# Kernel optimization log

Hardware: AMD Instinct MI355X
Metric: run time of the kernel (lower is better)

Reference implementation:

```python
import jax, jax.numpy as jnp
import numpy as np

ALPHA = 0.2  # LeakyReLU negative slope
NEG_INF = -9e15


def make_quaternion_mul(kernel):
    # kernel: (in/4, out); returns hamilton: (in, out)
    r, i, j, k = jnp.split(kernel, 4, axis=1)
    r2 = jnp.concatenate([r, -i, -j, -k], axis=0)
    i2 = jnp.concatenate([i, r, -k, j], axis=0)
    j2 = jnp.concatenate([j, k, r, -i], axis=0)
    k2 = jnp.concatenate([k, -j, i, r], axis=0)
    return jnp.concatenate([r2, i2, j2, k2], axis=1)


def setup_inputs() -> dict:
    key = jax.random.key(0)
    k1, k2, k3, k4 = jax.random.split(key, 4)
    N, IN, OUT, H = 4096, 512, 128, 4
    x = jax.random.normal(k1, (N, IN), dtype=jnp.float32)
    adj = jax.random.randint(k2, (N, N), 0, 2, dtype=jnp.int32)
    stdv = float(np.sqrt(6.0 / (IN // 4 + OUT)))
    W = jax.random.uniform(k3, (H, IN // 4, OUT), dtype=jnp.float32,
                           minval=-stdv, maxval=stdv)
    a_std = float(np.sqrt(2.0 / (2 * OUT + 1))) * 1.414
    a = jax.random.normal(k4, (H, 2 * OUT), dtype=jnp.float32) * a_std
    return {"x": x, "adj": adj, "W": W, "a": a}


def reference(x, adj, W, a):
    N = x.shape[0]
    hamilton = jax.vmap(make_quaternion_mul)(W)          # (H, IN, OUT)
    h = jnp.einsum('nf,hfo->hno', x, hamilton)           # (H, N, OUT)
    OUT = h.shape[-1]
    a_src, a_dst = a[:, :OUT], a[:, OUT:]
    # e[h,i,j] = leakyrelu(h_i . a_src + h_j . a_dst), same math as repeat/cat
    f_src = jnp.einsum('hno,ho->hn', h, a_src)           # (H, N)
    f_dst = jnp.einsum('hno,ho->hn', h, a_dst)           # (H, N)
    e = jax.nn.leaky_relu(f_src[:, :, None] + f_dst[:, None, :], ALPHA)
    e = jnp.where((adj > 0)[None, :, :], e, NEG_INF)
    attn = jax.nn.softmax(e, axis=-1)                    # (H, N, N)
    # dropout p=0.0 / eval mode -> identity
    h_prime = jnp.einsum('hnm,hmo->hno', attn, h)        # (H, N, OUT)
    out = jnp.transpose(h_prime, (1, 0, 2)).reshape(N, -1)  # concat heads
    return jax.nn.elu(out)
```

## Files before the change

### kernel.cpp

```cpp
#include <hip/hip_runtime.h>
#include <math.h>

#define ALPHA 0.2f

#define XS   544
#define HS   4128
#define HCS  66048

typedef __attribute__((ext_vector_type(8))) short short8;
typedef __attribute__((ext_vector_type(4))) float f32x4;
typedef __attribute__((ext_vector_type(4))) int i32x4;

__device__ __forceinline__ unsigned short f2bf(float f) {
    unsigned int x = __float_as_uint(f);
    x += 0x7fffu + ((x >> 16) & 1u);
    return (unsigned short)(x >> 16);
}
__device__ __forceinline__ unsigned int pack_rne(float lo, float hi) {
    return (unsigned int)f2bf(lo) | ((unsigned int)f2bf(hi) << 16);
}
__device__ __forceinline__ unsigned int pack_trunc(float lo, float hi) {
    return __builtin_amdgcn_perm(__float_as_uint(hi), __float_as_uint(lo), 0x07060302u);
}
__device__ __forceinline__ unsigned int bitmask1(unsigned int x, int j) {
    return (unsigned int)(((int)(x << (31 - j))) >> 31);
}

__global__ __launch_bounds__(256) void k_prep(const float* __restrict__ x,
                                              const float* __restrict__ W,
                                              const int* __restrict__ adj,
                                              unsigned short* __restrict__ xbf,
                                              unsigned short* __restrict__ hamT,
                                              unsigned int* __restrict__ adjp32) {
    const int b = blockIdx.x;
    if (b < 1024) {
        const int gid = b * 256 + threadIdx.x;
        const int row = gid >> 6, c8 = (gid & 63) * 8;
        const float4* xp = (const float4*)x + (size_t)gid * 2;
        const float4 f0 = xp[0], f1 = xp[1];
        const uint4 o = {pack_rne(f0.x, f0.y), pack_rne(f0.z, f0.w),
                         pack_rne(f1.x, f1.y), pack_rne(f1.z, f1.w)};
        *(uint4*)(xbf + (size_t)row * XS + c8) = o;
    } else if (b < 1152) {
        const int gid = (b - 1024) * 256 + threadIdx.x;
        const int head = gid >> 13;
        const int rem  = gid & 8191;
        const int o = rem >> 6, f8 = rem & 63;
        const int ob = o >> 5, oc = o & 31;
        float v[8];
#pragma unroll
        for (int j = 0; j < 8; j++) {
            const int f = f8 * 8 + j;
            const int bq = f >> 7, f0 = f & 127;
            const float s = ((0x5390u >> ((bq << 2) | ob)) & 1u) ? -1.0f : 1.0f;
            v[j] = s * W[(head << 14) + (f0 << 7) + (((bq ^ ob) << 5) | oc)];
        }
        const uint4 pk = {pack_rne(v[0], v[1]), pack_rne(v[2], v[3]),
                          pack_rne(v[4], v[5]), pack_rne(v[6], v[7])};
        *(uint4*)(hamT + (size_t)(head * 128 + o) * XS + f8 * 8) = pk;
    } else {
        const int gid = (b - 1152) * 256 + threadIdx.x;
        const int4* ap = (const int4*)(adj + (size_t)gid * 32);
        unsigned int u = 0;
#pragma unroll
        for (int q = 0; q < 8; q++) {
            const int4 v = ap[q];
            u |= (v.x > 0 ? 1u : 0u) << (q * 4);
            u |= (v.y > 0 ? 2u : 0u) << (q * 4);
            u |= (v.z > 0 ? 4u : 0u) << (q * 4);
            u |= (v.w > 0 ? 8u : 0u) << (q * 4);
        }
        adjp32[gid] = u;
    }
}

__global__ __launch_bounds__(256) void k_h(const unsigned short* __restrict__ xbf,
                                           const unsigned short* __restrict__ hamT,
                                           const float* __restrict__ a,
                                           unsigned short* __restrict__ hBT,
                                           float2* __restrict__ fsE,
                                           float2* __restrict__ fdE) {
    const int t = threadIdx.x;
    const int head = blockIdx.y;
    const int n0 = blockIdx.x * 64;
    const int wv = t >> 6, lane = t & 63;
    const int quad = lane >> 4, nl = lane & 15;
    const unsigned short* ap = xbf + (size_t)(n0 + wv * 16 + nl) * XS + quad * 8;
    const unsigned short* bp = hamT + (size_t)(head * 128 + nl) * XS + quad * 8;
    f32x4 acc[8];
#pragma unroll
    for (int ct = 0; ct < 8; ct++) acc[ct] = (f32x4){0.f, 0.f, 0.f, 0.f};
    for (int kc = 0; kc < 16; kc++) {
        const short8 af = *(const short8*)(ap + kc * 32);
#pragma unroll
        for (int ct = 0; ct < 8; ct++) {
            const short8 bf_ = *(const short8*)(bp + (size_t)ct * 16 * XS + kc * 32);
            acc[ct] = __builtin_amdgcn_mfma_f32_16x16x32_bf16(af, bf_, acc[ct], 0, 0, 0);
        }
    }
    const int rbase = n0 + wv * 16 + quad * 4;
#pragma unroll
    for (int ct = 0; ct < 8; ct++) {
        const uint2 pk = {pack_rne(acc[ct][0], acc[ct][1]), pack_rne(acc[ct][2], acc[ct][3])};
        *(uint2*)(hBT + (size_t)(head * 128 + ct * 16 + nl) * HS + rbase) = pk;
    }
    float fsr[4] = {0.f, 0.f, 0.f, 0.f}, fdr[4] = {0.f, 0.f, 0.f, 0.f};
#pragma unroll
    for (int ct = 0; ct < 8; ct++) {
        const int col = ct * 16 + nl;
        const float as = a[head * 256 + col];
        const float ad = a[head * 256 + 128 + col];
#pragma unroll
        for (int r = 0; r < 4; r++) {
            fsr[r] += acc[ct][r] * as;
            fdr[r] += acc[ct][r] * ad;
        }
    }
#pragma unroll
    for (int off = 1; off < 16; off <<= 1)
#pragma unroll
        for (int r = 0; r < 4; r++) {
            fsr[r] += __shfl_xor(fsr[r], off, 64);
            fdr[r] += __shfl_xor(fdr[r], off, 64);
        }
    if (nl == 0) {
#pragma unroll
        for (int r = 0; r < 4; r++) {
            const int n = rbase + r;
            fsE[(head << 12) + n] = make_float2(__expf(fsr[r]), __expf(ALPHA * fsr[r]));
            fdE[(head << 12) + n] = make_float2(__expf(fdr[r]), __expf(ALPHA * fdr[r]));
        }
    }
}

#define WELT(e1, ea, j, bits, es) \
    __uint_as_float(__float_as_uint(fmaxf((es).x * (e1), (es).y * (ea))) & bitmask1((bits), (j)))
#define WPK(f4, jb, bits, es) \
    pack_trunc(WELT((f4).x, (f4).y, (jb), (bits), (es)), \
               WELT((f4).z, (f4).w, (jb) + 1, (bits), (es)))

#define LOADM(S, mcn) do {                                                \
    const int _mo = (mcn) * 32;                                           \
    _Pragma("unroll")                                                     \
    for (int _ct = 0; _ct < 8; _ct++)                                     \
        Bst[S][_ct] = *(const short8*)(bbase + (size_t)_ct * HCS + _mo);  \
    _Pragma("unroll")                                                     \
    for (int _rt = 0; _rt < 4; _rt++) Kst[S][_rt] = ap[_rt][(mcn) * 4];   \
    _Pragma("unroll")                                                     \
    for (int _q = 0; _q < 4; _q++) Fst[S][_q] = fdb[(mcn) * 16 + _q];     \
} while (0)

#define EXECM(S) do {                                                     \
    short8 _af[4];                                                        \
    _Pragma("unroll")                                                     \
    for (int _rt = 0; _rt < 4; _rt++) {                                   \
        const i32x4 _ai = {(int)WPK(Fst[S][0], 0, Kst[S][_rt], es[_rt]),  \
                           (int)WPK(Fst[S][1], 2, Kst[S][_rt], es[_rt]),  \
                           (int)WPK(Fst[S][2], 4, Kst[S][_rt], es[_rt]),  \
                           (int)WPK(Fst[S][3], 6, Kst[S][_rt], es[_rt])}; \
        _af[_rt] = __builtin_bit_cast(short8, _ai);                       \
    }                                                                     \
    _Pragma("unroll")                                                     \
    for (int _rt = 0; _rt < 4; _rt++) {                                   \
        _Pragma("unroll")                                                 \
        for (int _ct = 0; _ct < 8; _ct++)                                 \
            acc[_rt][_ct] = __builtin_amdgcn_mfma_f32_16x16x32_bf16(      \
                _af[_rt], Bst[S][_ct], acc[_rt][_ct], 0, 0, 0);           \
        accL[_rt] = __builtin_amdgcn_mfma_f32_16x16x32_bf16(              \
            _af[_rt], ones, accL[_rt], 0, 0, 0);                          \
    }                                                                     \
} while (0)

__global__ __launch_bounds__(256, 1) void k_attn(const unsigned char* __restrict__ adjp,
                                                 const float2* __restrict__ fsE,
                                                 const float2* __restrict__ fdE,
                                                 const unsigned short* __restrict__ hBT,
                                                 float* __restrict__ out) {
    __shared__ f32x4 cbuf[1536];
    __shared__ f32x4 Lbuf[1024];
    const int t = threadIdx.x;
    const int head = blockIdx.x & 3;
    const int n0 = (blockIdx.x >> 2) * 64;
    const int wv = t >> 6, lane = t & 63;
    const int quad = lane >> 4, nl = lane & 15;
    const int m0base = wv << 10;
    float2 es[4];
    const unsigned char* ap[4];
#pragma unroll
    for (int rt = 0; rt < 4; rt++) {
        es[rt] = fsE[(head << 12) + n0 + rt * 16 + nl];
        ap[rt] = adjp + ((size_t)(n0 + rt * 16 + nl) << 9) + (m0base >> 3) + quad;
    }
    const float4* fdb = (const float4*)(fdE + (head << 12) + m0base + quad * 8);
    const unsigned short* bbase = hBT + (size_t)(head * 128 + nl) * HS + quad * 8 + m0base;
    const short8 ones = __builtin_bit_cast(short8,
        (i32x4){0x3F803F80, 0x3F803F80, 0x3F803F80, 0x3F803F80});
    f32x4 acc[4][8], accL[4];
#pragma unroll
    for (int rt = 0; rt < 4; rt++) {
        accL[rt] = (f32x4){0.f, 0.f, 0.f, 0.f};
#pragma unroll
        for (int ct = 0; ct < 8; ct++) acc[rt][ct] = (f32x4){0.f, 0.f, 0.f, 0.f};
    }
    short8 Bst[2][8];
    unsigned int Kst[2][4];
    float4 Fst[2][4];
    LOADM(0, 0);
    LOADM(1, 1);
    for (int mc = 0; mc < 32; mc += 2) {
        EXECM(0);
        LOADM(0, (mc + 2) & 31);
        EXECM(1);
        LOADM(1, (mc + 3) & 31);
    }
#pragma unroll
    for (int rt = 0; rt < 4; rt++) Lbuf[(wv * 4 + rt) * 64 + lane] = accL[rt];
#pragma unroll
    for (int rt = 0; rt < 4; rt++) {
        if (rt > 0) __syncthreads();
#pragma unroll
        for (int ct = 0; ct < 8; ct++) {
            const int owner = ct & 3;
            if (owner != wv) {
                const int j = (wv - owner - 1) & 3;
                cbuf[(ct * 3 + j) * 64 + lane] = acc[rt][ct];
            }
        }
        __syncthreads();
        f32x4 Lt = (f32x4){0.f, 0.f, 0.f, 0.f};
#pragma unroll
        for (int v = 0; v < 4; v++) Lt += Lbuf[(v * 4 + rt) * 64 + lane];
        float iL[4];
#pragma unroll
        for (int r = 0; r < 4; r++) iL[r] = (Lt[r] > 0.f) ? (1.0f / Lt[r]) : 0.0f;
#pragma unroll
        for (int ct = 0; ct < 8; ct++) {
            if ((ct & 3) == wv) {
                f32x4 tot = acc[rt][ct];
#pragma unroll
                for (int j = 0; j < 3; j++) tot += cbuf[(ct * 3 + j) * 64 + lane];
#pragma unroll
                for (int r = 0; r < 4; r++) {
                    float v = tot[r] * iL[r];
                    v = v > 0.f ? v : (__expf(v) - 1.0f);
                    out[(size_t)(n0 + rt * 16 + quad * 4 + r) * 512
                        + head * 128 + ct * 16 + nl] = v;
                }
            }
        }
    }
}

extern "C" void kernel_launch(void* const* d_in, const int* in_sizes, int n_in,
                              void* d_out, int out_size, void* d_ws, size_t ws_size,
                              hipStream_t stream) {
    (void)in_sizes; (void)n_in; (void)out_size; (void)ws_size;
    const float* x   = (const float*)d_in[0];
    const int*   adj = (const int*)d_in[1];
    const float* W   = (const float*)d_in[2];
    const float* a   = (const float*)d_in[3];
    float* out = (float*)d_out;

    char* ws = (char*)d_ws;
    unsigned short* xbf  = (unsigned short*)(ws);
    unsigned short* hBT  = (unsigned short*)(ws + 4456448);
    unsigned short* hamT = (unsigned short*)(ws + 8683520);
    unsigned char*  adjp = (unsigned char*)(ws + 9240576);
    float2*         fsE  = (float2*)(ws + 11337728);
    float2*         fdE  = (float2*)(ws + 11468800);

    hipLaunchKernelGGL(k_prep, dim3(3200),    dim3(256), 0, stream,
                       x, W, adj, xbf, hamT, (unsigned int*)adjp);
    hipLaunchKernelGGL(k_h,    dim3(64, 4),   dim3(256), 0, stream, xbf, hamT, a, hBT, fsE, fdE);
    hipLaunchKernelGGL(k_attn, dim3(256),     dim3(256), 0, stream, adjp, fsE, fdE, hBT, out);
}
```

Measured before the change: 159.8 us.

## Split attention key dimension across two blocks and combine partials in a new kernel

The attention kernel now splits the m (key) range into two halves, giving twice as many blocks (512 on the chip's 256 CUs) with launch bounds allowing two blocks per CU. Each half writes unnormalized partial sums and row-sum partials: one half writes into the output buffer, the other into workspace reused from the dead xbf region. A new combine kernel adds the partials, normalizes, and applies ELU. This aims to fix under-occupancy from having only 256 blocks, at the cost of an extra launch and roughly 16MB of extra global traffic.

```diff
diff --git a/kernel.cpp b/kernel.cpp
--- a/kernel.cpp
+++ b/kernel.cpp
@@ -171,19 +171,22 @@
     }                                                                     \
 } while (0)
 
-__global__ __launch_bounds__(256, 1) void k_attn(const unsigned char* __restrict__ adjp,
+__global__ __launch_bounds__(256, 2) void k_attn(const unsigned char* __restrict__ adjp,
                                                  const float2* __restrict__ fsE,
                                                  const float2* __restrict__ fdE,
                                                  const unsigned short* __restrict__ hBT,
-                                                 float* __restrict__ out) {
+                                                 float* __restrict__ out,
+                                                 float* __restrict__ pacc1,
+                                                 float* __restrict__ pL) {
     __shared__ f32x4 cbuf[1536];
     __shared__ f32x4 Lbuf[1024];
     const int t = threadIdx.x;
-    const int head = blockIdx.x & 3;
-    const int n0 = (blockIdx.x >> 2) * 64;
+    const int head  = blockIdx.x & 3;
+    const int mhalf = (blockIdx.x >> 2) & 1;
+    const int n0 = (blockIdx.x >> 3) * 64;
     const int wv = t >> 6, lane = t & 63;
     const int quad = lane >> 4, nl = lane & 15;
-    const int m0base = wv << 10;
+    const int m0base = mhalf * 2048 + (wv << 9);
     float2 es[4];
     const unsigned char* ap[4];
 #pragma unroll
@@ -207,12 +210,13 @@
     float4 Fst[2][4];
     LOADM(0, 0);
     LOADM(1, 1);
-    for (int mc = 0; mc < 32; mc += 2) {
+    for (int mc = 0; mc < 16; mc += 2) {
         EXECM(0);
-        LOADM(0, (mc + 2) & 31);
+        LOADM(0, (mc + 2) & 15);
         EXECM(1);
-        LOADM(1, (mc + 3) & 31);
-    }
+        LOADM(1, (mc + 3) & 15);
+    }
+    float* const pdst = (mhalf == 0) ? out : pacc1;
 #pragma unroll
     for (int rt = 0; rt < 4; rt++) Lbuf[(wv * 4 + rt) * 64 + lane] = accL[rt];
 #pragma unroll
@@ -227,12 +231,14 @@
             }
         }
         __syncthreads();
-        f32x4 Lt = (f32x4){0.f, 0.f, 0.f, 0.f};
-#pragma unroll
-        for (int v = 0; v < 4; v++) Lt += Lbuf[(v * 4 + rt) * 64 + lane];
-        float iL[4];
-#pragma unroll
-        for (int r = 0; r < 4; r++) iL[r] = (Lt[r] > 0.f) ? (1.0f / Lt[r]) : 0.0f;
+        if (wv == 0 && nl == 0) {
+            f32x4 Lt = (f32x4){0.f, 0.f, 0.f, 0.f};
+#pragma unroll
+            for (int v = 0; v < 4; v++) Lt += Lbuf[(v * 4 + rt) * 64 + lane];
+#pragma unroll
+            for (int r = 0; r < 4; r++)
+                pL[mhalf * 16384 + (head << 12) + n0 + rt * 16 + quad * 4 + r] = Lt[r];
+        }
 #pragma unroll
         for (int ct = 0; ct < 8; ct++) {
             if ((ct & 3) == wv) {
@@ -240,15 +246,32 @@
 #pragma unroll
                 for (int j = 0; j < 3; j++) tot += cbuf[(ct * 3 + j) * 64 + lane];
 #pragma unroll
-                for (int r = 0; r < 4; r++) {
-                    float v = tot[r] * iL[r];
-                    v = v > 0.f ? v : (__expf(v) - 1.0f);
-                    out[(size_t)(n0 + rt * 16 + quad * 4 + r) * 512
-                        + head * 128 + ct * 16 + nl] = v;
-                }
+                for (int r = 0; r < 4; r++)
+                    pdst[(size_t)(n0 + rt * 16 + quad * 4 + r) * 512
+                         + head * 128 + ct * 16 + nl] = tot[r];
             }
         }
     }
+}
+
+__global__ __launch_bounds__(256) void k_comb(const float* __restrict__ pacc1,
+                                              const float* __restrict__ pL,
+                                              float* __restrict__ out) {
+    const int gid = blockIdx.x * 256 + threadIdx.x;
+    const int c4 = gid & 127, row = gid >> 7;
+    const int head = c4 >> 5;
+    const size_t base = (size_t)row * 512 + c4 * 4;
+    const float4 t0 = *(const float4*)(out + base);
+    const float4 t1 = *(const float4*)(pacc1 + base);
+    const float L = pL[(head << 12) + row] + pL[16384 + (head << 12) + row];
+    const float iL = (L > 0.f) ? (1.0f / L) : 0.0f;
+    float4 o;
+    float v;
+    v = (t0.x + t1.x) * iL; o.x = v > 0.f ? v : (__expf(v) - 1.0f);
+    v = (t0.y + t1.y) * iL; o.y = v > 0.f ? v : (__expf(v) - 1.0f);
+    v = (t0.z + t1.z) * iL; o.z = v > 0.f ? v : (__expf(v) - 1.0f);
+    v = (t0.w + t1.w) * iL; o.w = v > 0.f ? v : (__expf(v) - 1.0f);
+    *(float4*)(out + base) = o;
 }
 
 extern "C" void kernel_launch(void* const* d_in, const int* in_sizes, int n_in,
@@ -262,15 +285,19 @@
     float* out = (float*)d_out;
 
     char* ws = (char*)d_ws;
-    unsigned short* xbf  = (unsigned short*)(ws);
-    unsigned short* hBT  = (unsigned short*)(ws + 4456448);
-    unsigned short* hamT = (unsigned short*)(ws + 8683520);
-    unsigned char*  adjp = (unsigned char*)(ws + 9240576);
-    float2*         fsE  = (float2*)(ws + 11337728);
-    float2*         fdE  = (float2*)(ws + 11468800);
+    unsigned short* hBT  = (unsigned short*)(ws);
+    unsigned char*  adjp = (unsigned char*)(ws + 4227072);
+    float2*         fsE  = (float2*)(ws + 6324224);
+    float2*         fdE  = (float2*)(ws + 6455296);
+    float*          pL   = (float*)(ws + 6586368);
+    unsigned short* xbf  = (unsigned short*)(ws + 6717440);
+    unsigned short* hamT = (unsigned short*)(ws + 11173888);
+    float*          pacc1 = (float*)(ws + 6717440);
 
     hipLaunchKernelGGL(k_prep, dim3(3200),    dim3(256), 0, stream,
                        x, W, adj, xbf, hamT, (unsigned int*)adjp);
     hipLaunchKernelGGL(k_h,    dim3(64, 4),   dim3(256), 0, stream, xbf, hamT, a, hBT, fsE, fdE);
-    hipLaunchKernelGGL(k_attn, dim3(256),     dim3(256), 0, stream, adjp, fsE, fdE, hBT, out);
-}
+    hipLaunchKernelGGL(k_attn, dim3(512),     dim3(256), 0, stream,
+                       adjp, fsE, fdE, hBT, out, pacc1, pL);
+    hipLaunchKernelGGL(k_comb, dim3(2048),    dim3(256), 0, stream, pacc1, pL, out);
+}
```

Result: slower. 210.6 us (+31.8%).

## Retile hBT into contiguous chunks and give each wave its own rows

Applied to the files above, without the earlier changes.

The h output is now stored in 32-node chunks so each B fragment load is a contiguous 1KB-stride access instead of a large-stride gather. Each wave in k_attn now owns 16 query rows and sweeps all 4096 keys, rather than splitting keys across waves. This removes the LDS cross-wave reduction, the shared buffers and the barriers of the epilogue. Per-wave register state shrinks from 4x8 to 8 accumulators, and launch_bounds no longer pins one block per CU, which may allow more occupancy. In exchange each wave runs four times as many loop iterations, and periodic __syncthreads calls are added, presumably to keep the waves in step so B loads can be shared through cache.

```diff
diff --git a/kernel.cpp b/kernel.cpp
--- a/kernel.cpp
+++ b/kernel.cpp
@@ -4,8 +4,6 @@
 #define ALPHA 0.2f
 
 #define XS   544
-#define HS   4128
-#define HCS  66048
 
 typedef __attribute__((ext_vector_type(8))) short short8;
 typedef __attribute__((ext_vector_type(4))) float f32x4;
@@ -99,10 +97,12 @@
         }
     }
     const int rbase = n0 + wv * 16 + quad * 4;
+    const int c = rbase >> 5, s = rbase & 31;
 #pragma unroll
     for (int ct = 0; ct < 8; ct++) {
         const uint2 pk = {pack_rne(acc[ct][0], acc[ct][1]), pack_rne(acc[ct][2], acc[ct][3])};
-        *(uint2*)(hBT + (size_t)(head * 128 + ct * 16 + nl) * HS + rbase) = pk;
+        *(uint2*)(hBT + (size_t)head * 524288 + (size_t)c * 4096
+                  + (ct * 16 + nl) * 32 + s) = pk;
     }
     float fsr[4] = {0.f, 0.f, 0.f, 0.f}, fdr[4] = {0.f, 0.f, 0.f, 0.f};
 #pragma unroll
@@ -139,114 +139,74 @@
     pack_trunc(WELT((f4).x, (f4).y, (jb), (bits), (es)), \
                WELT((f4).z, (f4).w, (jb) + 1, (bits), (es)))
 
-#define LOADM(S, mcn) do {                                                \
-    const int _mo = (mcn) * 32;                                           \
-    _Pragma("unroll")                                                     \
-    for (int _ct = 0; _ct < 8; _ct++)                                     \
-        Bst[S][_ct] = *(const short8*)(bbase + (size_t)_ct * HCS + _mo);  \
-    _Pragma("unroll")                                                     \
-    for (int _rt = 0; _rt < 4; _rt++) Kst[S][_rt] = ap[_rt][(mcn) * 4];   \
-    _Pragma("unroll")                                                     \
-    for (int _q = 0; _q < 4; _q++) Fst[S][_q] = fdb[(mcn) * 16 + _q];     \
+#define LOADM(S, mcn) do {                                                 \
+    const int _c = (mcn) & 127;                                            \
+    const unsigned short* _bb = hb + (size_t)_c * 4096;                    \
+    _Pragma("unroll")                                                      \
+    for (int _ct = 0; _ct < 8; _ct++)                                      \
+        Bst[S][_ct] = *(const short8*)(_bb + _ct * 512);                   \
+    Kst[S] = ap[_c * 4];                                                   \
+    _Pragma("unroll")                                                      \
+    for (int _q = 0; _q < 4; _q++) Fst[S][_q] = fdb[_c * 16 + _q];         \
 } while (0)
 
-#define EXECM(S) do {                                                     \
-    short8 _af[4];                                                        \
-    _Pragma("unroll")                                                     \
-    for (int _rt = 0; _rt < 4; _rt++) {                                   \
-        const i32x4 _ai = {(int)WPK(Fst[S][0], 0, Kst[S][_rt], es[_rt]),  \
-                           (int)WPK(Fst[S][1], 2, Kst[S][_rt], es[_rt]),  \
-                           (int)WPK(Fst[S][2], 4, Kst[S][_rt], es[_rt]),  \
-                           (int)WPK(Fst[S][3], 6, Kst[S][_rt], es[_rt])}; \
-        _af[_rt] = __builtin_bit_cast(short8, _ai);                       \
-    }                                                                     \
-    _Pragma("unroll")                                                     \
-    for (int _rt = 0; _rt < 4; _rt++) {                                   \
-        _Pragma("unroll")                                                 \
-        for (int _ct = 0; _ct < 8; _ct++)                                 \
-            acc[_rt][_ct] = __builtin_amdgcn_mfma_f32_16x16x32_bf16(      \
-                _af[_rt], Bst[S][_ct], acc[_rt][_ct], 0, 0, 0);           \
-        accL[_rt] = __builtin_amdgcn_mfma_f32_16x16x32_bf16(              \
-            _af[_rt], ones, accL[_rt], 0, 0, 0);                          \
-    }                                                                     \
+#define EXECM(S) do {                                                      \
+    const i32x4 _ai = {(int)WPK(Fst[S][0], 0, Kst[S], es),                 \
+                       (int)WPK(Fst[S][1], 2, Kst[S], es),                 \
+                       (int)WPK(Fst[S][2], 4, Kst[S], es),                 \
+                       (int)WPK(Fst[S][3], 6, Kst[S], es)};                \
+    const short8 _af = __builtin_bit_cast(short8, _ai);                    \
+    _Pragma("unroll")                                                      \
+    for (int _ct = 0; _ct < 8; _ct++)                                      \
+        acc[_ct] = __builtin_amdgcn_mfma_f32_16x16x32_bf16(                \
+            _af, Bst[S][_ct], acc[_ct], 0, 0, 0);                          \
+    accL = __builtin_amdgcn_mfma_f32_16x16x32_bf16(_af, ones, accL, 0, 0, 0); \
 } while (0)
 
-__global__ __launch_bounds__(256, 1) void k_attn(const unsigned char* __restrict__ adjp,
-                                                 const float2* __restrict__ fsE,
-                                                 const float2* __restrict__ fdE,
-                                                 const unsigned short* __restrict__ hBT,
-                                                 float* __restrict__ out) {
-    __shared__ f32x4 cbuf[1536];
-    __shared__ f32x4 Lbuf[1024];
+__global__ __launch_bounds__(256) void k_attn(const unsigned char* __restrict__ adjp,
+                                              const float2* __restrict__ fsE,
+                                              const float2* __restrict__ fdE,
+                                              const unsigned short* __restrict__ hBT,
+                                              float* __restrict__ out) {
     const int t = threadIdx.x;
     const int head = blockIdx.x & 3;
     const int n0 = (blockIdx.x >> 2) * 64;
     const int wv = t >> 6, lane = t & 63;
     const int quad = lane >> 4, nl = lane & 15;
-    const int m0base = wv << 10;
-    float2 es[4];
-    const unsigned char* ap[4];
-#pragma unroll
-    for (int rt = 0; rt < 4; rt++) {
-        es[rt] = fsE[(head << 12) + n0 + rt * 16 + nl];
-        ap[rt] = adjp + ((size_t)(n0 + rt * 16 + nl) << 9) + (m0base >> 3) + quad;
-    }
-    const float4* fdb = (const float4*)(fdE + (head << 12) + m0base + quad * 8);
-    const unsigned short* bbase = hBT + (size_t)(head * 128 + nl) * HS + quad * 8 + m0base;
+    const int row = n0 + wv * 16 + nl;
+    const float2 es = fsE[(head << 12) + row];
+    const unsigned char* ap = adjp + ((size_t)row << 9) + quad;
+    const float4* fdb = (const float4*)(fdE + (head << 12) + quad * 8);
+    const unsigned short* hb = hBT + (size_t)head * 524288 + nl * 32 + quad * 8;
     const short8 ones = __builtin_bit_cast(short8,
         (i32x4){0x3F803F80, 0x3F803F80, 0x3F803F80, 0x3F803F80});
-    f32x4 acc[4][8], accL[4];
-#pragma unroll
-    for (int rt = 0; rt < 4; rt++) {
-        accL[rt] = (f32x4){0.f, 0.f, 0.f, 0.f};
-#pragma unroll
-        for (int ct = 0; ct < 8; ct++) acc[rt][ct] = (f32x4){0.f, 0.f, 0.f, 0.f};
-    }
+    f32x4 acc[8], accL;
+    accL = (f32x4){0.f, 0.f, 0.f, 0.f};
+#pragma unroll
+    for (int ct = 0; ct < 8; ct++) acc[ct] = (f32x4){0.f, 0.f, 0.f, 0.f};
     short8 Bst[2][8];
-    unsigned int Kst[2][4];
+    unsigned int Kst[2];
     float4 Fst[2][4];
     LOADM(0, 0);
     LOADM(1, 1);
-    for (int mc = 0; mc < 32; mc += 2) {
+    for (int mc = 0; mc < 128; mc += 2) {
         EXECM(0);
-        LOADM(0, (mc + 2) & 31);
+        LOADM(0, mc + 2);
         EXECM(1);
-        LOADM(1, (mc + 3) & 31);
-    }
-#pragma unroll
-    for (int rt = 0; rt < 4; rt++) Lbuf[(wv * 4 + rt) * 64 + lane] = accL[rt];
-#pragma unroll
-    for (int rt = 0; rt < 4; rt++) {
-        if (rt > 0) __syncthreads();
-#pragma unroll
-        for (int ct = 0; ct < 8; ct++) {
-            const int owner = ct & 3;
-            if (owner != wv) {
-                const int j = (wv - owner - 1) & 3;
-                cbuf[(ct * 3 + j) * 64 + lane] = acc[rt][ct];
-            }
-        }
-        __syncthreads();
-        f32x4 Lt = (f32x4){0.f, 0.f, 0.f, 0.f};
-#pragma unroll
-        for (int v = 0; v < 4; v++) Lt += Lbuf[(v * 4 + rt) * 64 + lane];
-        float iL[4];
-#pragma unroll
-        for (int r = 0; r < 4; r++) iL[r] = (Lt[r] > 0.f) ? (1.0f / Lt[r]) : 0.0f;
-#pragma unroll
-        for (int ct = 0; ct < 8; ct++) {
-            if ((ct & 3) == wv) {
-                f32x4 tot = acc[rt][ct];
-#pragma unroll
-                for (int j = 0; j < 3; j++) tot += cbuf[(ct * 3 + j) * 64 + lane];
-#pragma unroll
-                for (int r = 0; r < 4; r++) {
-                    float v = tot[r] * iL[r];
-                    v = v > 0.f ? v : (__expf(v) - 1.0f);
-                    out[(size_t)(n0 + rt * 16 + quad * 4 + r) * 512
-                        + head * 128 + ct * 16 + nl] = v;
-                }
-            }
+        LOADM(1, mc + 3);
+        if ((mc & 15) == 14) __syncthreads();
+    }
+    float iL[4];
+#pragma unroll
+    for (int r = 0; r < 4; r++) iL[r] = (accL[r] > 0.f) ? (1.0f / accL[r]) : 0.0f;
+#pragma unroll
+    for (int ct = 0; ct < 8; ct++) {
+#pragma unroll
+        for (int r = 0; r < 4; r++) {
+            float v = acc[ct][r] * iL[r];
+            v = v > 0.f ? v : (__expf(v) - 1.0f);
+            out[(size_t)(n0 + wv * 16 + quad * 4 + r) * 512
+                + head * 128 + ct * 16 + nl] = v;
         }
     }
 }
@@ -262,15 +222,15 @@
     float* out = (float*)d_out;
 
     char* ws = (char*)d_ws;
-    unsigned short* xbf  = (unsigned short*)(ws);
-    unsigned short* hBT  = (unsigned short*)(ws + 4456448);
-    unsigned short* hamT = (unsigned short*)(ws + 8683520);
-    unsigned char*  adjp = (unsigned char*)(ws + 9240576);
-    float2*         fsE  = (float2*)(ws + 11337728);
-    float2*         fdE  = (float2*)(ws + 11468800);
-
-    hipLaunchKernelGGL(k_prep, dim3(3200),    dim3(256), 0, stream,
+    unsigned short* hBT  = (unsigned short*)(ws);
+    unsigned char*  adjp = (unsigned char*)(ws + 4194304);
+    float2*         fsE  = (float2*)(ws + 6291456);
+    float2*         fdE  = (float2*)(ws + 6422528);
+    unsigned short* xbf  = (unsigned short*)(ws + 6553600);
+    unsigned short* hamT = (unsigned short*)(ws + 11010048);
+
+    hipLaunchKernelGGL(k_prep, dim3(3200),  dim3(256), 0, stream,
                        x, W, adj, xbf, hamT, (unsigned int*)adjp);
-    hipLaunchKernelGGL(k_h,    dim3(64, 4),   dim3(256), 0, stream, xbf, hamT, a, hBT, fsE, fdE);
-    hipLaunchKernelGGL(k_attn, dim3(256),     dim3(256), 0, stream, adjp, fsE, fdE, hBT, out);
-}
+    hipLaunchKernelGGL(k_h,    dim3(64, 4), dim3(256), 0, stream, xbf, hamT, a, hBT, fsE, fdE);
+    hipLaunchKernelGGL(k_attn, dim3(256),   dim3(256), 0, stream, adjp, fsE, fdE, hBT, out);
+}
```

Measured after the change: 204.8 us. 1.28x slower.
